# Kernel tuning notes

Measured on AMD Instinct MI355X. Metric: run time of the kernel, lower is better.

Reference implementation:

```python
import jax, jax.numpy as jnp
import numpy as np


def _multinomial_sample(t, gumbel, k):
    # t: [R, S] non-negative weights (R = batch*hidden). Torch's
    # torch.multinomial(t, k) (without replacement) is distributionally
    # equivalent to top-k of log(t) + Gumbel noise (Gumbel top-k trick).
    row_sum = jnp.sum(t, axis=1, keepdims=True)          # [R, 1]
    mask = (row_sum == 0).astype(t.dtype)                # [R, 1]
    t = t + mask                                         # zero rows -> uniform
    scores = jnp.log(t) + gumbel                         # log(0) = -inf: never picked
    _, idx = jax.lax.top_k(scores, k)                    # [R, k] sampled w/o replacement
    vals = jnp.take_along_axis(t, idx, axis=1)           # gather sampled weights
    vals = vals + mask * (-1.0)                          # undo the +1 on masked rows
    return vals.sum(axis=1)                              # [R]


def setup_inputs() -> dict:
    key = jax.random.key(0)
    k1, k2, k3, k4 = jax.random.split(key, 4)
    B, S, H = 8, 4096, 1024
    hidden_states = jax.random.normal(k1, (B, S, H), dtype=jnp.float32)
    u = jax.random.uniform(k2, (B * H, S), dtype=jnp.float32, minval=1e-6, maxval=1.0)
    gumbel = -jnp.log(-jnp.log(u))
    W = jax.random.normal(k3, (H, H), dtype=jnp.float32) * 0.02
    b = jax.random.normal(k4, (H,), dtype=jnp.float32) * 0.02
    return {"hidden_states": hidden_states, "gumbel": gumbel, "W": W, "b": b, "sample": 8}


def reference(hidden_states, gumbel, W, b, sample):
    B, S, H = hidden_states.shape
    rep = jax.nn.relu(hidden_states)                     # [B, S, H]
    t = rep.transpose(0, 2, 1).reshape(-1, S)            # [B*H, S]
    pooled = _multinomial_sample(t, gumbel, sample).reshape(B, H)
    out = pooled @ W.T + b                               # nn.Linear(H, H)
    return jnp.tanh(out)
```

## Files before the change

kernel.cpp:

```cpp
#include <hip/hip_runtime.h>
#include <math.h>

#define BB 8
#define SS 4096
#define HH 1024
#define ROWS (BB * HH)
#define KTOP 8
#define NS 32
#define SC (SS / NS)
#define SCW (SC / 4)

#define INSERTD(D, XD) do {                                               \
    const double _x = (XD);                                               \
    const double _n0 = fmax(D[0], _x);                                    \
    const double _n1 = fmax(D[1], fmin(D[0], _x));                        \
    const double _n2 = fmax(D[2], fmin(D[1], _x));                        \
    const double _n3 = fmax(D[3], fmin(D[2], _x));                        \
    const double _n4 = fmax(D[4], fmin(D[3], _x));                        \
    const double _n5 = fmax(D[5], fmin(D[4], _x));                        \
    const double _n6 = fmax(D[6], fmin(D[5], _x));                        \
    const double _n7 = fmax(D[7], fmin(D[6], _x));                        \
    D[0] = _n0; D[1] = _n1; D[2] = _n2; D[3] = _n3;                       \
    D[4] = _n4; D[5] = _n5; D[6] = _n6; D[7] = _n7;                       \
  } while (0)

__global__ __launch_bounds__(256) void topk_partial(
    const float* __restrict__ hidden, const float* __restrict__ gumbel,
    double* __restrict__ pairs) {
  __shared__ double lst[256 * 9];

  const int tid = threadIdx.x;
  const int rl  = tid & 63;
  const int w   = tid >> 6;
  const int sc  = blockIdx.x;
  const int rb  = blockIdx.y;
  const int r   = rb * 64 + rl;
  const int b   = rb >> 4;
  const int h0  = (rb & 15) << 6;
  const int s_base = sc * SC + w * SCW;

  const float4* __restrict__ gp =
      (const float4*)(gumbel + (size_t)r * SS + s_base);
  const float* __restrict__ hp =
      hidden + ((size_t)b * SS + s_base) * HH + h0 + rl;

  float4 g[8];
#pragma unroll
  for (int i = 0; i < 8; ++i) g[i] = gp[i];
  float hv[32];
#pragma unroll
  for (int i = 0; i < 32; ++i) hv[i] = hp[(size_t)i * HH];

  double D[8];
#pragma unroll
  for (int i = 0; i < KTOP; ++i) D[i] = -(double)INFINITY;

#pragma unroll
  for (int k = 0; k < 8; ++k) {
    const float gg[4] = {g[k].x, g[k].y, g[k].z, g[k].w};
#pragma unroll
    for (int c = 0; c < 4; ++c) {
      const float t   = fmaxf(hv[k * 4 + c], 0.0f);
      const float scv = logf(t) + gg[c];
      double xd = (double)scv;
      xd = __longlong_as_double(__double_as_longlong(xd)
             | (long long)(__float_as_uint(t) >> 2));
      INSERTD(D, xd);
    }
  }

#pragma unroll
  for (int j = 0; j < KTOP; ++j) lst[(w * 64 + rl) * 9 + j] = D[j];
  __syncthreads();
  if (w == 0 || w == 2) {
#pragma unroll
    for (int j = 0; j < KTOP; ++j) {
      const double xd = lst[((w + 1) * 64 + rl) * 9 + j];
      INSERTD(D, xd);
    }
    if (w == 2) {
#pragma unroll
      for (int j = 0; j < KTOP; ++j) lst[(2 * 64 + rl) * 9 + j] = D[j];
    }
  }
  __syncthreads();
  if (w == 0) {
#pragma unroll
    for (int j = 0; j < KTOP; ++j) {
      const double xd = lst[(2 * 64 + rl) * 9 + j];
      INSERTD(D, xd);
    }
    double* __restrict__ op = pairs + ((size_t)r * NS + sc) * KTOP;
#pragma unroll
    for (int j = 0; j < KTOP; ++j) op[j] = D[j];
  }
}

__global__ __launch_bounds__(256) void topk_merge(
    const double* __restrict__ pairs, float* __restrict__ pooled) {
  __shared__ double ls[256 * 9];
  const int tid  = threadIdx.x;
  const int rloc = tid >> 3;
  const int q    = tid & 7;
  const int r    = blockIdx.x * 32 + rloc;
  const int slot = rloc * 8 + q;

  double D[8];
#pragma unroll
  for (int i = 0; i < KTOP; ++i) D[i] = -(double)INFINITY;

  const int cpg = NS / 8;
  const double2* __restrict__ p =
      (const double2*)(pairs + ((size_t)r * NS + q * cpg) * KTOP);
#pragma unroll
  for (int i = 0; i < cpg * KTOP / 2; ++i) {
    const double2 two = p[i];
    INSERTD(D, two.x);
    INSERTD(D, two.y);
  }
#pragma unroll
  for (int j = 0; j < KTOP; ++j) ls[slot * 9 + j] = D[j];
  __syncthreads();
  if ((q & 1) == 0) {
#pragma unroll
    for (int j = 0; j < KTOP; ++j) {
      const double xd = ls[(slot + 1) * 9 + j];
      INSERTD(D, xd);
    }
#pragma unroll
    for (int j = 0; j < KTOP; ++j) ls[slot * 9 + j] = D[j];
  }
  __syncthreads();
  if ((q & 3) == 0) {
#pragma unroll
    for (int j = 0; j < KTOP; ++j) {
      const double xd = ls[(slot + 2) * 9 + j];
      INSERTD(D, xd);
    }
#pragma unroll
    for (int j = 0; j < KTOP; ++j) ls[slot * 9 + j] = D[j];
  }
  __syncthreads();
  if (q == 0) {
#pragma unroll
    for (int j = 0; j < KTOP; ++j) {
      const double xd = ls[(slot + 4) * 9 + j];
      INSERTD(D, xd);
    }
    float sum = 0.0f;
#pragma unroll
    for (int j = 0; j < KTOP; ++j) {
      const unsigned int lo = (unsigned int)__double_as_longlong(D[j]);
      sum += __uint_as_float((lo & 0x1FFFFFFFu) << 2);
    }
    pooled[r] = sum;
  }
}

__global__ __launch_bounds__(256) void linear_tanh(
    const float* __restrict__ pooled, const float* __restrict__ W,
    const float* __restrict__ bias, float* __restrict__ out) {
  __shared__ float lp[ROWS];
  const int tid = threadIdx.x;
#pragma unroll
  for (int i = 0; i < ROWS / 4 / 256; ++i)
    ((float4*)lp)[i * 256 + tid] = ((const float4*)pooled)[i * 256 + tid];
  __syncthreads();

  const int wave = tid >> 6;
  const int lane = tid & 63;
  const int j = blockIdx.x * 4 + wave;

  float acc[BB];
#pragma unroll
  for (int bb = 0; bb < BB; ++bb) acc[bb] = 0.0f;
#pragma unroll
  for (int k0 = 0; k0 < HH; k0 += 256) {
    const float4 w4 = *(const float4*)&W[(size_t)j * HH + k0 + lane * 4];
#pragma unroll
    for (int bb = 0; bb < BB; ++bb) {
      const float4 p4 = *(const float4*)&lp[bb * HH + k0 + lane * 4];
      acc[bb] += w4.x * p4.x + w4.y * p4.y + w4.z * p4.z + w4.w * p4.w;
    }
  }
#pragma unroll
  for (int bb = 0; bb < BB; ++bb) {
    float a = acc[bb];
    for (int off = 32; off > 0; off >>= 1) a += __shfl_down(a, off, 64);
    if (lane == 0) out[(size_t)bb * HH + j] = tanhf(a + bias[j]);
  }
}

extern "C" void kernel_launch(void* const* d_in, const int* in_sizes, int n_in,
                              void* d_out, int out_size, void* d_ws, size_t ws_size,
                              hipStream_t stream) {
  const float* hidden = (const float*)d_in[0];
  const float* gumbel = (const float*)d_in[1];
  const float* W      = (const float*)d_in[2];
  const float* bias   = (const float*)d_in[3];
  float* out          = (float*)d_out;

  double* pairs  = (double*)d_ws;
  float*  pooled = (float*)((char*)d_ws
                   + (size_t)ROWS * NS * KTOP * sizeof(double));

  topk_partial<<<dim3(NS, ROWS / 64), dim3(256), 0, stream>>>(hidden, gumbel, pairs);
  topk_merge<<<dim3(ROWS / 32), dim3(256), 0, stream>>>(pairs, pooled);
  linear_tanh<<<dim3(HH / 4), dim3(256), 0, stream>>>(pooled, W, bias, out);
}
```

Baseline: 308.1 us.

## Stage topk inputs via direct global-to-LDS loads and widen merge parallelism

The partial top-k kernel now issues 16-byte global_load_lds transfers that place the gumbel and hidden tiles straight into a 64KB LDS buffer. It then consumes them in four chunks, each gated by a partial vmcnt wait, so arithmetic on early chunks can overlap the remaining loads and register pressure drops. Hidden loads are re-laid so each lane fetches 16 contiguous bytes instead of scalar strided loads. The merge kernel uses 16 threads per row with an extra reduction level and twice as many blocks. The 64KB of LDS per block limits occupancy and relies on hand-counted vmcnt values.

```diff
diff --git a/kernel.cpp b/kernel.cpp
--- a/kernel.cpp
+++ b/kernel.cpp
@@ -24,10 +24,19 @@
     D[4] = _n4; D[5] = _n5; D[6] = _n6; D[7] = _n7;                       \
   } while (0)
 
+#define AS1 __attribute__((address_space(1)))
+#define AS3 __attribute__((address_space(3)))
+static __device__ __forceinline__ void stage16(const float* g, float* l) {
+  __builtin_amdgcn_global_load_lds((AS1 const void*)g, (AS3 void*)l, 16, 0, 0);
+}
+
 __global__ __launch_bounds__(256) void topk_partial(
     const float* __restrict__ hidden, const float* __restrict__ gumbel,
     double* __restrict__ pairs) {
-  __shared__ double lst[256 * 9];
+  __shared__ __align__(16) char smem[65536];
+  float* const h_lds = (float*)smem;
+  float* const g_lds = (float*)(smem + 32768);
+  double* const lst  = (double*)smem;
 
   const int tid = threadIdx.x;
   const int rl  = tid & 63;
@@ -37,38 +46,60 @@
   const int r   = rb * 64 + rl;
   const int b   = rb >> 4;
   const int h0  = (rb & 15) << 6;
-  const int s_base = sc * SC + w * SCW;
-
-  const float4* __restrict__ gp =
-      (const float4*)(gumbel + (size_t)r * SS + s_base);
-  const float* __restrict__ hp =
-      hidden + ((size_t)b * SS + s_base) * HH + h0 + rl;
-
-  float4 g[8];
-#pragma unroll
-  for (int i = 0; i < 8; ++i) g[i] = gp[i];
-  float hv[32];
-#pragma unroll
-  for (int i = 0; i < 32; ++i) hv[i] = hp[(size_t)i * HH];
+  const int s_w0 = sc * SC + w * SCW;
+
+  const float* gsrc = gumbel + (size_t)r * SS + s_w0;
+  const float* hsrc = hidden + ((size_t)b * SS + s_w0) * HH + h0 + ((rl & 15) << 2);
+  const int hs_lane = rl >> 4;
+
+  float* const gdst = g_lds + w * (8 * 64 * 4);
+  float* const hdst = h_lds + w * (32 * 64);
+
+#pragma unroll
+  for (int q = 0; q < 4; ++q) {
+#pragma unroll
+    for (int ii = 0; ii < 2; ++ii) {
+      const int i = q * 2 + ii;
+      stage16(gsrc + i * 4, gdst + i * 256);
+    }
+#pragma unroll
+    for (int ii = 0; ii < 2; ++ii) {
+      const int i = q * 2 + ii;
+      stage16(hsrc + (size_t)(i * 4 + hs_lane) * HH, hdst + i * 256);
+    }
+  }
 
   double D[8];
 #pragma unroll
   for (int i = 0; i < KTOP; ++i) D[i] = -(double)INFINITY;
 
-#pragma unroll
-  for (int k = 0; k < 8; ++k) {
-    const float gg[4] = {g[k].x, g[k].y, g[k].z, g[k].w};
-#pragma unroll
-    for (int c = 0; c < 4; ++c) {
-      const float t   = fmaxf(hv[k * 4 + c], 0.0f);
-      const float scv = logf(t) + gg[c];
-      double xd = (double)scv;
-      xd = __longlong_as_double(__double_as_longlong(xd)
-             | (long long)(__float_as_uint(t) >> 2));
-      INSERTD(D, xd);
-    }
-  }
-
+  const float* const grd = gdst + (rl << 2);
+  const float* const hrd = hdst + rl;
+
+#pragma unroll
+  for (int q = 0; q < 4; ++q) {
+    if (q == 0)      asm volatile("s_waitcnt vmcnt(12)" ::: "memory");
+    else if (q == 1) asm volatile("s_waitcnt vmcnt(8)"  ::: "memory");
+    else if (q == 2) asm volatile("s_waitcnt vmcnt(4)"  ::: "memory");
+    else             asm volatile("s_waitcnt vmcnt(0)"  ::: "memory");
+    __builtin_amdgcn_sched_barrier(0);
+#pragma unroll
+    for (int ii = 0; ii < 2; ++ii) {
+      const int i = q * 2 + ii;
+      const float4 gg = *(const float4*)(grd + i * 256);
+#pragma unroll
+      for (int c = 0; c < 4; ++c) {
+        const float t   = fmaxf(hrd[(i * 4 + c) * 64], 0.0f);
+        const float scv = logf(t) + ((const float*)&gg)[c];
+        double xd = (double)scv;
+        xd = __longlong_as_double(__double_as_longlong(xd)
+               | (long long)(__float_as_uint(t) >> 2));
+        INSERTD(D, xd);
+      }
+    }
+  }
+
+  __syncthreads();
 #pragma unroll
   for (int j = 0; j < KTOP; ++j) lst[(w * 64 + rl) * 9 + j] = D[j];
   __syncthreads();
@@ -100,16 +131,16 @@
     const double* __restrict__ pairs, float* __restrict__ pooled) {
   __shared__ double ls[256 * 9];
   const int tid  = threadIdx.x;
-  const int rloc = tid >> 3;
-  const int q    = tid & 7;
-  const int r    = blockIdx.x * 32 + rloc;
-  const int slot = rloc * 8 + q;
+  const int rloc = tid >> 4;
+  const int q    = tid & 15;
+  const int r    = blockIdx.x * 16 + rloc;
+  const int slot = tid;
 
   double D[8];
 #pragma unroll
   for (int i = 0; i < KTOP; ++i) D[i] = -(double)INFINITY;
 
-  const int cpg = NS / 8;
+  const int cpg = NS / 16;
   const double2* __restrict__ p =
       (const double2*)(pairs + ((size_t)r * NS + q * cpg) * KTOP);
 #pragma unroll
@@ -123,30 +154,28 @@
   __syncthreads();
   if ((q & 1) == 0) {
 #pragma unroll
-    for (int j = 0; j < KTOP; ++j) {
-      const double xd = ls[(slot + 1) * 9 + j];
-      INSERTD(D, xd);
-    }
+    for (int j = 0; j < KTOP; ++j) INSERTD(D, ls[(slot + 1) * 9 + j]);
 #pragma unroll
     for (int j = 0; j < KTOP; ++j) ls[slot * 9 + j] = D[j];
   }
   __syncthreads();
   if ((q & 3) == 0) {
 #pragma unroll
-    for (int j = 0; j < KTOP; ++j) {
-      const double xd = ls[(slot + 2) * 9 + j];
-      INSERTD(D, xd);
-    }
+    for (int j = 0; j < KTOP; ++j) INSERTD(D, ls[(slot + 2) * 9 + j]);
 #pragma unroll
     for (int j = 0; j < KTOP; ++j) ls[slot * 9 + j] = D[j];
   }
   __syncthreads();
+  if ((q & 7) == 0) {
+#pragma unroll
+    for (int j = 0; j < KTOP; ++j) INSERTD(D, ls[(slot + 4) * 9 + j]);
+#pragma unroll
+    for (int j = 0; j < KTOP; ++j) ls[slot * 9 + j] = D[j];
+  }
+  __syncthreads();
   if (q == 0) {
 #pragma unroll
-    for (int j = 0; j < KTOP; ++j) {
-      const double xd = ls[(slot + 4) * 9 + j];
-      INSERTD(D, xd);
-    }
+    for (int j = 0; j < KTOP; ++j) INSERTD(D, ls[(slot + 8) * 9 + j]);
     float sum = 0.0f;
 #pragma unroll
     for (int j = 0; j < KTOP; ++j) {
@@ -205,6 +234,6 @@
                    + (size_t)ROWS * NS * KTOP * sizeof(double));
 
   topk_partial<<<dim3(NS, ROWS / 64), dim3(256), 0, stream>>>(hidden, gumbel, pairs);
-  topk_merge<<<dim3(ROWS / 32), dim3(256), 0, stream>>>(pairs, pooled);
+  topk_merge<<<dim3(ROWS / 16), dim3(256), 0, stream>>>(pairs, pooled);
   linear_tanh<<<dim3(HH / 4), dim3(256), 0, stream>>>(pooled, W, bias, out);
 }
```

After: 312.6 us. Within noise of the previous version (+1.5%).
